# Performance work log

Hardware: AMD Instinct MI355X
Metric: run time of the kernel (lower is better)

Reference implementation:

```python
import jax, jax.numpy as jnp
import numpy as np


def setup_inputs() -> dict:
    key = jax.random.key(0)
    ks = jax.random.split(key, 6)
    Q, S, D, C = 128, 512, 768, 64
    return {
        "query_reps": jax.random.normal(ks[0], (Q, D), dtype=jnp.float32),
        "support_reps": jax.random.normal(ks[1], (S, D), dtype=jnp.float32),
        "W1": jax.random.normal(ks[2], (2 * D, 2 * D), dtype=jnp.float32) * 0.02,
        "b1": jnp.zeros((2 * D,), dtype=jnp.float32),
        "W2": jax.random.normal(ks[3], (1, 2 * D), dtype=jnp.float32) * 0.02,
        "b2": jnp.zeros((1,), dtype=jnp.float32),
        "support_labels": jnp.sort(jax.random.randint(ks[4], (S,), 0, C)),
        "query_target_ids": jax.random.randint(ks[5], (Q,), 0, C),
        "num_classes": C,
    }


def reference(query_reps, support_reps, W1, b1, W2, b2,
              support_labels, query_target_ids, num_classes):
    D = query_reps.shape[1]
    # Original: concat_reps = cat([repeat_interleave(q, S), s.repeat(Q)], dim=1)
    # then relu(Linear_2Dx2D(concat)). Equivalent split-weight form avoids the
    # explicit [Q*S, 2D] concat: x @ W1.T = q @ W1[:, :D].T + s @ W1[:, D:].T
    hq = query_reps @ W1[:, :D].T        # [Q, 2D]
    hs = support_reps @ W1[:, D:].T      # [S, 2D]
    h = jax.nn.relu(hq[:, None, :] + hs[None, :, :] + b1)   # [Q, S, 2D]
    scores = jnp.einsum('qsd,d->qs', h, W2[0]) + b2[0]       # [Q, S]
    # aggregate_scores_by_label with support_reduction='score':
    # M one-hot [C, S] row-normalized (p=1) => per-label mean of scores.
    seg = jax.ops.segment_sum(scores.T, support_labels,
                              num_segments=num_classes).T     # [Q, C]
    counts = jax.ops.segment_sum(jnp.ones((support_labels.shape[0],), jnp.float32),
                                 support_labels, num_segments=num_classes)
    agg = seg / jnp.maximum(counts, 1.0)                      # [Q, C]
    logp = jax.nn.log_softmax(agg, axis=1)
    loss = -jnp.mean(jnp.take_along_axis(logp, query_target_ids[:, None], axis=1))
    preds = jnp.argmax(agg, axis=1)
    return (loss, preds == query_target_ids)
```

## Files before the change

kernel.cpp:

```cpp
#include <hip/hip_runtime.h>
#include <math.h>

#define QN 128
#define SN 512
#define DN 768
#define TDN 1536
#define CN 64
#define KSPLIT 4
#define KCH 192

#define HQP_ELEMS (KSPLIT * QN * TDN)
#define HSP_ELEMS (KSPLIT * SN * TDN)
#define ZERO_ELEMS (QN * CN)

typedef short short8 __attribute__((ext_vector_type(8)));
typedef float f32x4 __attribute__((ext_vector_type(4)));

#define LDS_STRIDE 40
#define PLANE (128 * LDS_STRIDE)

__device__ __forceinline__ short bf16_rtn(float x) {
    unsigned u = __float_as_uint(x);
    return (short)((u + 0x7fffu + ((u >> 16) & 1u)) >> 16);
}
__device__ __forceinline__ float bf16_tof(short s) {
    return __uint_as_float(((unsigned)(unsigned short)s) << 16);
}

__global__ __launch_bounds__(256) void gemm_kernel(
    const float* __restrict__ query, const float* __restrict__ support,
    const float* __restrict__ W1, float* __restrict__ hqp, float* __restrict__ hsp,
    float* __restrict__ zbuf, float* __restrict__ out)
{
    const int nt = blockIdx.x;
    const int mt = blockIdx.y;
    const int kz = blockIdx.z;
    const int tid = threadIdx.x;

    if (nt == 0 && kz == 0) {
        int o = (mt * 256 + tid) * 8;
        if (o < ZERO_ELEMS) {
            *(float4*)&zbuf[o]     = make_float4(0.f, 0.f, 0.f, 0.f);
            *(float4*)&zbuf[o + 4] = make_float4(0.f, 0.f, 0.f, 0.f);
        }
        if (mt == 0 && tid == 0) out[0] = 0.0f;
    }

    const float* A;
    float* Cout;
    int M0, Koff;
    if (mt == 0) { A = query;   M0 = 0;              Koff = 0;  Cout = hqp + (size_t)kz * QN * TDN; }
    else         { A = support; M0 = (mt - 1) * 128; Koff = DN; Cout = hsp + (size_t)kz * SN * TDN; }

    __shared__ short lds[2][4][PLANE];

    const int r  = tid >> 1;
    const int kh = (tid & 1) * 16;

    const float* Arow = &A [(size_t)(M0 + r) * DN  + kz * KCH + kh];
    const float* Brow = &W1[(size_t)(nt * 128 + r) * TDN + Koff + kz * KCH + kh];

    f32x4 acc[4][4];
    #pragma unroll
    for (int i = 0; i < 4; ++i)
        #pragma unroll
        for (int j = 0; j < 4; ++j)
            acc[i][j] = (f32x4){0.f, 0.f, 0.f, 0.f};

    auto stage = [&](short* plane, float4 v0, float4 v1, float4 v2, float4 v3) {
        float f[16] = {v0.x,v0.y,v0.z,v0.w, v1.x,v1.y,v1.z,v1.w,
                       v2.x,v2.y,v2.z,v2.w, v3.x,v3.y,v3.z,v3.w};
        short hi[16], lo[16];
        #pragma unroll
        for (int i = 0; i < 16; ++i) {
            hi[i] = bf16_rtn(f[i]);
            lo[i] = bf16_rtn(f[i] - bf16_tof(hi[i]));
        }
        short* dsth = plane + r * LDS_STRIDE + kh;
        #pragma unroll
        for (int i = 0; i < 16; ++i) dsth[i] = hi[i];
        short* dstl = plane + PLANE + r * LDS_STRIDE + kh;
        #pragma unroll
        for (int i = 0; i < 16; ++i) dstl[i] = lo[i];
    };

    {
        float4 a0 = *(const float4*)(Arow),     a1 = *(const float4*)(Arow + 4);
        float4 a2 = *(const float4*)(Arow + 8), a3 = *(const float4*)(Arow + 12);
        float4 b0 = *(const float4*)(Brow),     b1 = *(const float4*)(Brow + 4);
        float4 b2 = *(const float4*)(Brow + 8), b3 = *(const float4*)(Brow + 12);
        stage(lds[0][0], a0, a1, a2, a3);
        stage(lds[0][2], b0, b1, b2, b3);
    }
    __syncthreads();

    const int lane  = tid & 63;
    const int w     = tid >> 6;
    const int lm    = lane & 15;
    const int quad  = lane >> 4;
    const int wrow0 = (w >> 1) * 64;
    const int wcol0 = (w & 1) * 64;

    int buf = 0;
    for (int step = 0; step < 6; ++step) {
        float4 a0, a1, a2, a3, b0, b1, b2, b3;
        if (step < 5) {
            const float* An = Arow + (step + 1) * 32;
            const float* Bn = Brow + (step + 1) * 32;
            a0 = *(const float4*)(An);     a1 = *(const float4*)(An + 4);
            a2 = *(const float4*)(An + 8); a3 = *(const float4*)(An + 12);
            b0 = *(const float4*)(Bn);     b1 = *(const float4*)(Bn + 4);
            b2 = *(const float4*)(Bn + 8); b3 = *(const float4*)(Bn + 12);
        }

        const short* Ah = lds[buf][0];
        const short* Al = lds[buf][1];
        const short* Bh = lds[buf][2];
        const short* Bl = lds[buf][3];

        short8 ah[4], al[4], bh[4], bl[4];
        #pragma unroll
        for (int mi = 0; mi < 4; ++mi) {
            int off = (wrow0 + mi * 16 + lm) * LDS_STRIDE + quad * 8;
            ah[mi] = *(const short8*)&Ah[off];
            al[mi] = *(const short8*)&Al[off];
        }
        #pragma unroll
        for (int ni = 0; ni < 4; ++ni) {
            int off = (wcol0 + ni * 16 + lm) * LDS_STRIDE + quad * 8;
            bh[ni] = *(const short8*)&Bh[off];
            bl[ni] = *(const short8*)&Bl[off];
        }
        #pragma unroll
        for (int mi = 0; mi < 4; ++mi)
            #pragma unroll
            for (int ni = 0; ni < 4; ++ni) {
                acc[mi][ni] = __builtin_amdgcn_mfma_f32_16x16x32_bf16(ah[mi], bh[ni], acc[mi][ni], 0, 0, 0);
                acc[mi][ni] = __builtin_amdgcn_mfma_f32_16x16x32_bf16(ah[mi], bl[ni], acc[mi][ni], 0, 0, 0);
                acc[mi][ni] = __builtin_amdgcn_mfma_f32_16x16x32_bf16(al[mi], bh[ni], acc[mi][ni], 0, 0, 0);
            }

        if (step < 5) {
            int nb = buf ^ 1;
            stage(lds[nb][0], a0, a1, a2, a3);
            stage(lds[nb][2], b0, b1, b2, b3);
            __syncthreads();
            buf = nb;
        }
    }

    #pragma unroll
    for (int mi = 0; mi < 4; ++mi)
        #pragma unroll
        for (int ni = 0; ni < 4; ++ni) {
            int grow = M0 + wrow0 + mi * 16 + quad * 4;
            int gcol = nt * 128 + wcol0 + ni * 16 + lm;
            #pragma unroll
            for (int rr = 0; rr < 4; ++rr)
                Cout[(size_t)(grow + rr) * TDN + gcol] = acc[mi][ni][rr];
        }
}

__global__ __launch_bounds__(256) void score_kernel(
    const float* __restrict__ hqp, const float* __restrict__ hsp,
    const float* __restrict__ b1, const float* __restrict__ W2,
    const int* __restrict__ labels, float* __restrict__ aggbuf)
{
    const int jc = blockIdx.x;
    const int qt = blockIdx.y;
    const int st = blockIdx.z;

    __shared__ float hqT[96][64];
    __shared__ float hsT[96][64];
    __shared__ float w2s[96];
    __shared__ float sc[64][68];
    __shared__ int   lab[64];

    const int tid = threadIdx.x;
    if (tid < 64) lab[tid] = labels[st * 64 + tid];

    #pragma unroll
    for (int l = 0; l < 6; ++l) {
        int idx  = tid + l * 256;
        int row  = idx / 24;
        int quad = idx - row * 24;
        int j    = jc * 96 + quad * 4;
        float4 hv = *(const float4*)&b1[j];
        float4 sv = make_float4(0.f, 0.f, 0.f, 0.f);
        #pragma unroll
        for (int p = 0; p < KSPLIT; ++p) {
            float4 h = *(const float4*)&hqp[(size_t)p * QN * TDN + (size_t)(qt * 64 + row) * TDN + j];
            float4 g = *(const float4*)&hsp[(size_t)p * SN * TDN + (size_t)(st * 64 + row) * TDN + j];
            hv.x += h.x; hv.y += h.y; hv.z += h.z; hv.w += h.w;
            sv.x += g.x; sv.y += g.y; sv.z += g.z; sv.w += g.w;
        }
        hqT[quad*4+0][row] = hv.x; hqT[quad*4+1][row] = hv.y;
        hqT[quad*4+2][row] = hv.z; hqT[quad*4+3][row] = hv.w;
        hsT[quad*4+0][row] = sv.x; hsT[quad*4+1][row] = sv.y;
        hsT[quad*4+2][row] = sv.z; hsT[quad*4+3][row] = sv.w;
    }
    if (tid < 24) {
        float4 w = *(const float4*)&W2[jc * 96 + tid * 4];
        w2s[tid*4+0] = w.x; w2s[tid*4+1] = w.y;
        w2s[tid*4+2] = w.z; w2s[tid*4+3] = w.w;
    }
    __syncthreads();

    const int tx = tid & 15;
    const int ty = tid >> 4;
    float acc[4][4];
    #pragma unroll
    for (int i = 0; i < 4; ++i)
        #pragma unroll
        for (int j = 0; j < 4; ++j) acc[i][j] = 0.0f;

    #pragma unroll 4
    for (int jj = 0; jj < 96; ++jj) {
        float4 a4 = *(const float4*)&hqT[jj][ty * 4];
        float4 b4 = *(const float4*)&hsT[jj][tx * 4];
        float w = w2s[jj];
        float a[4] = {a4.x, a4.y, a4.z, a4.w};
        float b[4] = {b4.x, b4.y, b4.z, b4.w};
        #pragma unroll
        for (int i = 0; i < 4; ++i)
            #pragma unroll
            for (int j = 0; j < 4; ++j)
                acc[i][j] += w * fmaxf(a[i] + b[j], 0.0f);
    }

    #pragma unroll
    for (int i = 0; i < 4; ++i)
        *(float4*)&sc[ty * 4 + i][tx * 4] =
            make_float4(acc[i][0], acc[i][1], acc[i][2], acc[i][3]);
    __syncthreads();

    {
        int row = tid >> 2;
        int seg = tid & 3;
        float* aggrow = aggbuf + (size_t)(qt * 64 + row) * CN;
        int   runc = lab[seg * 16];
        float runv = 0.0f;
        #pragma unroll
        for (int k = 0; k < 16; ++k) {
            int s = seg * 16 + k;
            int c = lab[s];
            if (c != runc) { atomicAdd(&aggrow[runc], runv); runv = 0.0f; runc = c; }
            runv += sc[row][s];
        }
        atomicAdd(&aggrow[runc], runv);
    }
}

__global__ __launch_bounds__(256) void finale_kernel(
    const float* __restrict__ aggbuf, const int* __restrict__ labels,
    const int* __restrict__ tgt, float* __restrict__ out)
{
    __shared__ float cnt[CN];
    const int tid = threadIdx.x;
    if (tid < CN) cnt[tid] = 0.0f;
    __syncthreads();
    atomicAdd(&cnt[labels[tid]],       1.0f);
    atomicAdd(&cnt[labels[tid + 256]], 1.0f);
    __syncthreads();

    const int lane = tid & 63;
    const int q    = blockIdx.x * 4 + (tid >> 6);

    float v = aggbuf[(size_t)q * CN + lane] / fmaxf(cnt[lane], 1.0f);
    float av = v; int am = lane;
    #pragma unroll
    for (int off = 1; off < 64; off <<= 1) {
        float ov = __shfl_xor(av, off);
        int   oi = __shfl_xor(am, off);
        if (ov > av || (ov == av && oi < am)) { av = ov; am = oi; }
    }
    float m = av;
    float e = expf(v - m);
    #pragma unroll
    for (int off = 1; off < 64; off <<= 1)
        e += __shfl_xor(e, off);
    int t = tgt[q];
    float vt = __shfl(v, t, 64);
    if (lane == 0) {
        out[1 + q] = (am == t) ? 1.0f : 0.0f;
        atomicAdd(&out[0], -(vt - m - logf(e)) / (float)QN);
    }
}

extern "C" void kernel_launch(void* const* d_in, const int* in_sizes, int n_in,
                              void* d_out, int out_size, void* d_ws, size_t ws_size,
                              hipStream_t stream) {
    const float* query   = (const float*)d_in[0];
    const float* support = (const float*)d_in[1];
    const float* W1      = (const float*)d_in[2];
    const float* b1      = (const float*)d_in[3];
    const float* W2      = (const float*)d_in[4];
    const int* labels = (const int*)d_in[6];
    const int* tgt    = (const int*)d_in[7];

    float* ws     = (float*)d_ws;
    float* hqp    = ws;
    float* hsp    = hqp + HQP_ELEMS;
    float* aggbuf = hsp + HSP_ELEMS;
    float* out    = (float*)d_out;

    hipLaunchKernelGGL(gemm_kernel, dim3(12, 5, 4), dim3(256), 0, stream,
                       query, support, W1, hqp, hsp, aggbuf, out);
    hipLaunchKernelGGL(score_kernel, dim3(16, 2, 8), dim3(256), 0, stream,
                       hqp, hsp, b1, W2, labels, aggbuf);
    hipLaunchKernelGGL(finale_kernel, dim3(32), dim3(256), 0, stream,
                       aggbuf, labels, tgt, out);
}
```

Before: 120.0 us.

## Pre-split inputs to bf16 hi/lo and stream into LDS via global_load_lds

Adds a convert kernel that splits query, support and W1 once into bf16 hi/lo arrays in workspace. The GEMM then fills LDS with direct global-to-LDS 16-byte loads instead of converting in registers, so each block no longer redoes the fp32-to-bf16 split. The cost is an extra kernel launch, extra global traffic for the bf16 copies, and an unpadded LDS stride of 32 that may cause bank conflicts.

```diff
diff --git a/kernel.cpp b/kernel.cpp
--- a/kernel.cpp
+++ b/kernel.cpp
@@ -9,6 +9,11 @@
 #define KSPLIT 4
 #define KCH 192
 
+#define A_ROWS 640
+#define A_FLOATS (A_ROWS * DN)
+#define B_FLOATS (TDN * TDN)
+#define Q_FLOATS (QN * DN)
+
 #define HQP_ELEMS (KSPLIT * QN * TDN)
 #define HSP_ELEMS (KSPLIT * SN * TDN)
 #define ZERO_ELEMS (QN * CN)
@@ -16,9 +21,6 @@
 typedef short short8 __attribute__((ext_vector_type(8)));
 typedef float f32x4 __attribute__((ext_vector_type(4)));
 
-#define LDS_STRIDE 40
-#define PLANE (128 * LDS_STRIDE)
-
 __device__ __forceinline__ short bf16_rtn(float x) {
     unsigned u = __float_as_uint(x);
     return (short)((u + 0x7fffu + ((u >> 16) & 1u)) >> 16);
@@ -27,38 +29,74 @@
     return __uint_as_float(((unsigned)(unsigned short)s) << 16);
 }
 
+__device__ __forceinline__ void gload_lds16(const short* g, short* l) {
+    __builtin_amdgcn_global_load_lds(
+        (const __attribute__((address_space(1))) void*)g,
+        (__attribute__((address_space(3))) void*)l,
+        16, 0, 0);
+}
+
+__global__ __launch_bounds__(256) void convert_kernel(
+    const float* __restrict__ query, const float* __restrict__ support,
+    const float* __restrict__ W1,
+    short* __restrict__ Ah, short* __restrict__ Al,
+    short* __restrict__ Bh, short* __restrict__ Bl,
+    float* __restrict__ zbuf, float* __restrict__ out)
+{
+    const int flat = blockIdx.x * 256 + threadIdx.x;
+    if (blockIdx.x < 8) {
+        *(float4*)&zbuf[flat * 4] = make_float4(0.f, 0.f, 0.f, 0.f);
+        if (flat == 0) out[0] = 0.0f;
+    }
+    const long long i8 = (long long)flat * 8;
+    const float* src;
+    short *dh, *dl;
+    if (i8 < A_FLOATS) {
+        src = (i8 < Q_FLOATS) ? (query + i8) : (support + (i8 - Q_FLOATS));
+        dh = Ah + i8; dl = Al + i8;
+    } else {
+        long long o = i8 - A_FLOATS;
+        src = W1 + o; dh = Bh + o; dl = Bl + o;
+    }
+    float4 v0 = *(const float4*)src;
+    float4 v1 = *(const float4*)(src + 4);
+    float f[8] = {v0.x, v0.y, v0.z, v0.w, v1.x, v1.y, v1.z, v1.w};
+    short8 hi, lo;
+    #pragma unroll
+    for (int i = 0; i < 8; ++i) {
+        short h = bf16_rtn(f[i]);
+        hi[i] = h;
+        lo[i] = bf16_rtn(f[i] - bf16_tof(h));
+    }
+    *(short8*)dh = hi;
+    *(short8*)dl = lo;
+}
+
 __global__ __launch_bounds__(256) void gemm_kernel(
-    const float* __restrict__ query, const float* __restrict__ support,
-    const float* __restrict__ W1, float* __restrict__ hqp, float* __restrict__ hsp,
-    float* __restrict__ zbuf, float* __restrict__ out)
+    const short* __restrict__ Ah, const short* __restrict__ Al,
+    const short* __restrict__ Bh, const short* __restrict__ Bl,
+    float* __restrict__ hqp, float* __restrict__ hsp)
 {
     const int nt = blockIdx.x;
     const int mt = blockIdx.y;
     const int kz = blockIdx.z;
-    const int tid = threadIdx.x;
-
-    if (nt == 0 && kz == 0) {
-        int o = (mt * 256 + tid) * 8;
-        if (o < ZERO_ELEMS) {
-            *(float4*)&zbuf[o]     = make_float4(0.f, 0.f, 0.f, 0.f);
-            *(float4*)&zbuf[o + 4] = make_float4(0.f, 0.f, 0.f, 0.f);
-        }
-        if (mt == 0 && tid == 0) out[0] = 0.0f;
-    }
-
-    const float* A;
-    float* Cout;
-    int M0, Koff;
-    if (mt == 0) { A = query;   M0 = 0;              Koff = 0;  Cout = hqp + (size_t)kz * QN * TDN; }
-    else         { A = support; M0 = (mt - 1) * 128; Koff = DN; Cout = hsp + (size_t)kz * SN * TDN; }
-
-    __shared__ short lds[2][4][PLANE];
-
-    const int r  = tid >> 1;
-    const int kh = (tid & 1) * 16;
-
-    const float* Arow = &A [(size_t)(M0 + r) * DN  + kz * KCH + kh];
-    const float* Brow = &W1[(size_t)(nt * 128 + r) * TDN + Koff + kz * KCH + kh];
+    const int tid  = threadIdx.x;
+    const int lane = tid & 63;
+    const int w    = tid >> 6;
+
+    __shared__ short lds[2][4][128 * 32];
+
+    const int Koff = (mt == 0) ? 0 : DN;
+    float* Cout = (mt == 0)
+        ? (hqp + (size_t)kz * QN * TDN)
+        : (hsp + (size_t)kz * SN * TDN + (size_t)(mt - 1) * 128 * TDN);
+
+    const short* G;
+    int rs, grow0, gcol0;
+    if (w < 2) { G = (w == 0) ? Ah : Al; rs = DN;  grow0 = mt * 128; gcol0 = kz * KCH; }
+    else       { G = (w == 2) ? Bh : Bl; rs = TDN; grow0 = nt * 128; gcol0 = Koff + kz * KCH; }
+    const short* gsrc = G + (size_t)(grow0 + (lane >> 2)) * rs + gcol0 + (lane & 3) * 8;
+    const size_t cstride = (size_t)16 * rs;
 
     f32x4 acc[4][4];
     #pragma unroll
@@ -67,35 +105,14 @@
         for (int j = 0; j < 4; ++j)
             acc[i][j] = (f32x4){0.f, 0.f, 0.f, 0.f};
 
-    auto stage = [&](short* plane, float4 v0, float4 v1, float4 v2, float4 v3) {
-        float f[16] = {v0.x,v0.y,v0.z,v0.w, v1.x,v1.y,v1.z,v1.w,
-                       v2.x,v2.y,v2.z,v2.w, v3.x,v3.y,v3.z,v3.w};
-        short hi[16], lo[16];
-        #pragma unroll
-        for (int i = 0; i < 16; ++i) {
-            hi[i] = bf16_rtn(f[i]);
-            lo[i] = bf16_rtn(f[i] - bf16_tof(hi[i]));
-        }
-        short* dsth = plane + r * LDS_STRIDE + kh;
-        #pragma unroll
-        for (int i = 0; i < 16; ++i) dsth[i] = hi[i];
-        short* dstl = plane + PLANE + r * LDS_STRIDE + kh;
-        #pragma unroll
-        for (int i = 0; i < 16; ++i) dstl[i] = lo[i];
-    };
-
     {
-        float4 a0 = *(const float4*)(Arow),     a1 = *(const float4*)(Arow + 4);
-        float4 a2 = *(const float4*)(Arow + 8), a3 = *(const float4*)(Arow + 12);
-        float4 b0 = *(const float4*)(Brow),     b1 = *(const float4*)(Brow + 4);
-        float4 b2 = *(const float4*)(Brow + 8), b3 = *(const float4*)(Brow + 12);
-        stage(lds[0][0], a0, a1, a2, a3);
-        stage(lds[0][2], b0, b1, b2, b3);
-    }
-    __syncthreads();
-
-    const int lane  = tid & 63;
-    const int w     = tid >> 6;
+        short* lb = &lds[0][w][0];
+        #pragma unroll
+        for (int c = 0; c < 8; ++c)
+            gload_lds16(gsrc + c * cstride, lb + c * 512);
+    }
+    __syncthreads();
+
     const int lm    = lane & 15;
     const int quad  = lane >> 4;
     const int wrow0 = (w >> 1) * 64;
@@ -103,33 +120,31 @@
 
     int buf = 0;
     for (int step = 0; step < 6; ++step) {
-        float4 a0, a1, a2, a3, b0, b1, b2, b3;
         if (step < 5) {
-            const float* An = Arow + (step + 1) * 32;
-            const float* Bn = Brow + (step + 1) * 32;
-            a0 = *(const float4*)(An);     a1 = *(const float4*)(An + 4);
-            a2 = *(const float4*)(An + 8); a3 = *(const float4*)(An + 12);
-            b0 = *(const float4*)(Bn);     b1 = *(const float4*)(Bn + 4);
-            b2 = *(const float4*)(Bn + 8); b3 = *(const float4*)(Bn + 12);
-        }
-
-        const short* Ah = lds[buf][0];
-        const short* Al = lds[buf][1];
-        const short* Bh = lds[buf][2];
-        const short* Bl = lds[buf][3];
+            short* lb = &lds[buf ^ 1][w][0];
+            const short* gs = gsrc + (step + 1) * 32;
+            #pragma unroll
+            for (int c = 0; c < 8; ++c)
+                gload_lds16(gs + c * cstride, lb + c * 512);
+        }
+
+        const short* Ahs = &lds[buf][0][0];
+        const short* Als = &lds[buf][1][0];
+        const short* Bhs = &lds[buf][2][0];
+        const short* Bls = &lds[buf][3][0];
 
         short8 ah[4], al[4], bh[4], bl[4];
         #pragma unroll
         for (int mi = 0; mi < 4; ++mi) {
-            int off = (wrow0 + mi * 16 + lm) * LDS_STRIDE + quad * 8;
-            ah[mi] = *(const short8*)&Ah[off];
-            al[mi] = *(const short8*)&Al[off];
+            int off = (wrow0 + mi * 16 + lm) * 32 + quad * 8;
+            ah[mi] = *(const short8*)&Ahs[off];
+            al[mi] = *(const short8*)&Als[off];
         }
         #pragma unroll
         for (int ni = 0; ni < 4; ++ni) {
-            int off = (wcol0 + ni * 16 + lm) * LDS_STRIDE + quad * 8;
-            bh[ni] = *(const short8*)&Bh[off];
-            bl[ni] = *(const short8*)&Bl[off];
+            int off = (wcol0 + ni * 16 + lm) * 32 + quad * 8;
+            bh[ni] = *(const short8*)&Bhs[off];
+            bl[ni] = *(const short8*)&Bls[off];
         }
         #pragma unroll
         for (int mi = 0; mi < 4; ++mi)
@@ -140,20 +155,15 @@
                 acc[mi][ni] = __builtin_amdgcn_mfma_f32_16x16x32_bf16(al[mi], bh[ni], acc[mi][ni], 0, 0, 0);
             }
 
-        if (step < 5) {
-            int nb = buf ^ 1;
-            stage(lds[nb][0], a0, a1, a2, a3);
-            stage(lds[nb][2], b0, b1, b2, b3);
-            __syncthreads();
-            buf = nb;
-        }
+        __syncthreads();
+        buf ^= 1;
     }
 
     #pragma unroll
     for (int mi = 0; mi < 4; ++mi)
         #pragma unroll
         for (int ni = 0; ni < 4; ++ni) {
-            int grow = M0 + wrow0 + mi * 16 + quad * 4;
+            int grow = wrow0 + mi * 16 + quad * 4;
             int gcol = nt * 128 + wcol0 + ni * 16 + lm;
             #pragma unroll
             for (int rr = 0; rr < 4; ++rr)
@@ -302,10 +312,16 @@
     float* hqp    = ws;
     float* hsp    = hqp + HQP_ELEMS;
     float* aggbuf = hsp + HSP_ELEMS;
+    short* Ah     = (short*)(aggbuf + ZERO_ELEMS);
+    short* Al     = Ah + A_FLOATS;
+    short* Bh     = Al + A_FLOATS;
+    short* Bl     = Bh + B_FLOATS;
     float* out    = (float*)d_out;
 
+    hipLaunchKernelGGL(convert_kernel, dim3(1392), dim3(256), 0, stream,
+                       query, support, W1, Ah, Al, Bh, Bl, aggbuf, out);
     hipLaunchKernelGGL(gemm_kernel, dim3(12, 5, 4), dim3(256), 0, stream,
-                       query, support, W1, hqp, hsp, aggbuf, out);
+                       Ah, Al, Bh, Bl, hqp, hsp);
     hipLaunchKernelGGL(score_kernel, dim3(16, 2, 8), dim3(256), 0, stream,
                        hqp, hsp, b1, W2, labels, aggbuf);
     hipLaunchKernelGGL(finale_kernel, dim3(32), dim3(256), 0, stream,
```

Result: no change. 119.9 us (-0.0%).
